# Kernel optimization log

Measured on AMD Instinct MI355X. Metric: run time of the kernel, lower is better.

The kernel has to match this reference:

```python
import jax, jax.numpy as jnp
import numpy as np

NUM_HEADS = 16
D_MODEL = 1024
NEG_INF = -1e30


def setup_inputs() -> dict:
    key = jax.random.key(0)
    ks = jax.random.split(key, 7)
    B, S, D = 2, 2048, D_MODEL
    scale = 1.0 / np.sqrt(D)
    return {
        "queries": jax.random.normal(ks[0], (B, S, D), dtype=jnp.float32),
        "keys": jax.random.normal(ks[1], (B, S, D), dtype=jnp.float32),
        "values": jax.random.normal(ks[2], (B, S, D), dtype=jnp.float32),
        "Wq": jax.random.normal(ks[3], (D, D), dtype=jnp.float32) * scale,
        "Wk": jax.random.normal(ks[4], (D, D), dtype=jnp.float32) * scale,
        "Wv": jax.random.normal(ks[5], (D, D), dtype=jnp.float32) * scale,
        "Wo": jax.random.normal(ks[6], (D, D), dtype=jnp.float32) * scale,
    }


def _split_heads(x, h):
    # [B, S, D] -> [B, h, S, D/h]
    B, S, D = x.shape
    return x.reshape(B, S, h, D // h).transpose(0, 2, 1, 3)


def reference(queries, keys, values, Wq, Wk, Wv, Wo):
    h = NUM_HEADS
    q = _split_heads(queries @ Wq, h)  # [B, h, S, dh]
    k = _split_heads(keys @ Wk, h)
    v = _split_heads(values @ Wv, h)
    dh = q.shape[-1]
    scores = jnp.einsum("bhqd,bhkd->bhqk", q, k) / jnp.sqrt(jnp.float32(dh))
    # original quirk: exactly-zero scores are masked to -1e30 before softmax
    scores = jnp.where(scores == 0, NEG_INF, scores)
    attn = jax.nn.softmax(scores, axis=-1)
    out = jnp.einsum("bhqk,bhkd->bhqd", attn, v)  # [B, h, S, dh]
    B, _, S, _ = out.shape
    out = out.transpose(0, 2, 1, 3).reshape(B, S, h * dh)
    return out @ Wo
```

## Files before the change

### kernel.cpp

```cpp
#include <hip/hip_runtime.h>
#include <math.h>

typedef unsigned short u16;
typedef short bf16x8 __attribute__((ext_vector_type(8)));
typedef float f32x4 __attribute__((ext_vector_type(4)));

namespace {

constexpr int kB = 2, kS = 2048, kD = 1024, kH = 16, kDh = 64;

__device__ inline u16 f32_bf16(float f) {
    unsigned u = __float_as_uint(f);
    u += 0x7FFFu + ((u >> 16) & 1u);
    return (u16)(u >> 16);
}

__device__ inline u16 f32_bf16_fast(float f) {
    return (u16)((__float_as_uint(f) + 0x8000u) >> 16);
}

__device__ inline void gl_lds16(const void* g, void* l) {
    __builtin_amdgcn_global_load_lds(
        (const __attribute__((address_space(1))) void*)g,
        (__attribute__((address_space(3))) void*)l, 16, 0, 0);
}

__global__ __launch_bounds__(256) void conv_bf16_3(
    const float* __restrict__ s0, const float* __restrict__ s1,
    const float* __restrict__ s2,
    u16* __restrict__ d0, u16* __restrict__ d1, u16* __restrict__ d2)
{
    const int z = blockIdx.y;
    const float* src = z == 0 ? s0 : (z == 1 ? s1 : s2);
    u16* dst = z == 0 ? d0 : (z == 1 ? d1 : d2);
    const int i = blockIdx.x * 256 + threadIdx.x;
    const float4* s4 = (const float4*)src;
    float4 a = s4[2 * i], b = s4[2 * i + 1];
    uint4 o;
    o.x = (unsigned)f32_bf16(a.x) | ((unsigned)f32_bf16(a.y) << 16);
    o.y = (unsigned)f32_bf16(a.z) | ((unsigned)f32_bf16(a.w) << 16);
    o.z = (unsigned)f32_bf16(b.x) | ((unsigned)f32_bf16(b.y) << 16);
    o.w = (unsigned)f32_bf16(b.z) | ((unsigned)f32_bf16(b.w) << 16);
    ((uint4*)dst)[i] = o;
}

__global__ __launch_bounds__(256) void wtrans4(
    const float* __restrict__ W0, const float* __restrict__ W1,
    const float* __restrict__ W2, const float* __restrict__ W3,
    u16* __restrict__ T0, u16* __restrict__ T1,
    u16* __restrict__ T2, u16* __restrict__ T3)
{
    const int z = blockIdx.z;
    const float* W = z == 0 ? W0 : (z == 1 ? W1 : (z == 2 ? W2 : W3));
    u16* Wt = z == 0 ? T0 : (z == 1 ? T1 : (z == 2 ? T2 : T3));

    __shared__ __attribute__((aligned(16))) u16 T[64][65];
    const int t = threadIdx.x;
    const int n0 = blockIdx.x * 64, k0 = blockIdx.y * 64;
    const int r = t >> 4, c4 = (t & 15) * 4;
#pragma unroll
    for (int it = 0; it < 4; ++it) {
        const int rr = r + 16 * it;
        float4 v = *(const float4*)(W + (size_t)(k0 + rr) * kD + n0 + c4);
        T[rr][c4 + 0] = f32_bf16(v.x);
        T[rr][c4 + 1] = f32_bf16(v.y);
        T[rr][c4 + 2] = f32_bf16(v.z);
        T[rr][c4 + 3] = f32_bf16(v.w);
    }
    __syncthreads();
#pragma unroll
    for (int it = 0; it < 4; ++it) {
        const int nn = r + 16 * it;
        uint2 pk;
        pk.x = (unsigned)T[c4 + 0][nn] | ((unsigned)T[c4 + 1][nn] << 16);
        pk.y = (unsigned)T[c4 + 2][nn] | ((unsigned)T[c4 + 3][nn] << 16);
        *(uint2*)(Wt + (size_t)(n0 + nn) * kD + k0 + c4) = pk;
    }
}

__global__ __launch_bounds__(256) void vtrans(
    const u16* __restrict__ V, u16* __restrict__ Vt)
{
    __shared__ __attribute__((aligned(16))) u16 T[64][65];
    const int t = threadIdx.x;
    const int s0 = blockIdx.x * 64;
    const int bh = blockIdx.y, b = bh >> 4, h = bh & 15;
    const int rr = t >> 3, c0 = (t & 7) * 8;
    union { u16 u[8]; uint4 v4; } buf;
#pragma unroll
    for (int p = 0; p < 2; ++p) {
        const int s = rr + 32 * p;
        buf.v4 = *(const uint4*)(V + (size_t)(b * kS + s0 + s) * kD + h * kDh + c0);
#pragma unroll
        for (int i = 0; i < 8; ++i) T[c0 + i][s] = buf.u[i];
    }
    __syncthreads();
#pragma unroll
    for (int p = 0; p < 2; ++p) {
        const int d = rr + 32 * p;
#pragma unroll
        for (int i = 0; i < 8; ++i) buf.u[i] = T[d][c0 + i];
        *(uint4*)(Vt + (size_t)(bh * kDh + d) * kS + s0 + c0) = buf.v4;
    }
}

template <bool F32OUT>
__device__ inline void gemm_body(
    const u16* __restrict__ A, const u16* __restrict__ Wt,
    void* __restrict__ Cout, int M, int N, int K, int bx, int by)
{
    __shared__ __attribute__((aligned(16))) u16 As[64 * 32];
    __shared__ __attribute__((aligned(16))) u16 Bs[128 * 32];
    const int t = threadIdx.x, w = t >> 6, l = t & 63;
    const int quad = l >> 4, c = l & 15;
    const int m0 = by * 64, n0 = bx * 128;
    const int lr = l >> 2, lc = (l & 3) * 8;

    const u16* ga  = A  + (size_t)(m0 + w * 16 + lr) * K + lc;
    const u16* gb0 = Wt + (size_t)(n0 + w * 16 + lr) * K + lc;
    const u16* gb1 = Wt + (size_t)(n0 + 64 + w * 16 + lr) * K + lc;
    u16* lda  = &As[w * 512];
    u16* ldb0 = &Bs[w * 512];
    u16* ldb1 = &Bs[2048 + w * 512];

    const int fa = c * 32 + quad * 8;
    const int fb = (w * 32 + c) * 32 + quad * 8;

    f32x4 acc[4][2];
#pragma unroll
    for (int mi = 0; mi < 4; ++mi)
#pragma unroll
        for (int nj = 0; nj < 2; ++nj) acc[mi][nj] = 0;

    for (int k0 = 0; k0 < K; k0 += 32) {
        gl_lds16(ga + k0, lda);
        gl_lds16(gb0 + k0, ldb0);
        gl_lds16(gb1 + k0, ldb1);
        __syncthreads();
        bf16x8 af[4], bf[2];
#pragma unroll
        for (int mi = 0; mi < 4; ++mi) af[mi] = *(const bf16x8*)&As[fa + mi * 512];
#pragma unroll
        for (int nj = 0; nj < 2; ++nj) bf[nj] = *(const bf16x8*)&Bs[fb + nj * 512];
#pragma unroll
        for (int mi = 0; mi < 4; ++mi)
#pragma unroll
            for (int nj = 0; nj < 2; ++nj)
                acc[mi][nj] = __builtin_amdgcn_mfma_f32_16x16x32_bf16(
                    af[mi], bf[nj], acc[mi][nj], 0, 0, 0);
        __syncthreads();
    }

#pragma unroll
    for (int mi = 0; mi < 4; ++mi)
#pragma unroll
        for (int nj = 0; nj < 2; ++nj)
#pragma unroll
            for (int r = 0; r < 4; ++r) {
                const size_t row = m0 + mi * 16 + quad * 4 + r;
                const size_t col = n0 + w * 32 + nj * 16 + c;
                if (F32OUT)
                    ((float*)Cout)[row * N + col] = acc[mi][nj][r];
                else
                    ((u16*)Cout)[row * N + col] = f32_bf16(acc[mi][nj][r]);
            }
}

__global__ __launch_bounds__(256) void gemm_qkv(
    const u16* __restrict__ A0, const u16* __restrict__ A1,
    const u16* __restrict__ A2,
    const u16* __restrict__ W0, const u16* __restrict__ W1,
    const u16* __restrict__ W2,
    u16* __restrict__ C0, u16* __restrict__ C1, u16* __restrict__ C2)
{
    const int z = blockIdx.z;
    const u16* A  = z == 0 ? A0 : (z == 1 ? A1 : A2);
    const u16* Wt = z == 0 ? W0 : (z == 1 ? W1 : W2);
    u16* C = z == 0 ? C0 : (z == 1 ? C1 : C2);
    gemm_body<false>(A, Wt, C, kB * kS, kD, kD, blockIdx.x, blockIdx.y);
}

__global__ __launch_bounds__(256) void gemm_out(
    const u16* __restrict__ A, const u16* __restrict__ Wt,
    float* __restrict__ C)
{
    gemm_body<true>(A, Wt, C, kB * kS, kD, kD, blockIdx.x, blockIdx.y);
}

__global__ __launch_bounds__(256) void attn(
    const u16* __restrict__ Q, const u16* __restrict__ K,
    const u16* __restrict__ Vt, u16* __restrict__ AO)
{
    __shared__ __attribute__((aligned(16))) u16 KsL[2 * 64 * 32];
    __shared__ __attribute__((aligned(16))) u16 VtL[2 * 64 * 32];
    __shared__ __attribute__((aligned(16))) u16 QPs[9216];

    const int t = threadIdx.x, w = t >> 6, l = t & 63;
    const int quad = l >> 4, c = l & 15;
    const int q0 = blockIdx.x * 128;
    const int bh = blockIdx.y, b = bh >> 4, h = bh & 15;
    const int lr = l >> 2, lc8 = (l & 3) * 8;

    const size_t qbase = (size_t)(b * kS + q0) * kD + h * kDh;
#pragma unroll
    for (int p = 0; p < 2; ++p)
#pragma unroll
        for (int hf = 0; hf < 2; ++hf) {
            const int r0 = w * 32 + hf * 16;
            gl_lds16(Q + qbase + (size_t)(r0 + lr) * kD + p * 32 + lc8,
                     &QPs[p * 4096 + r0 * 32]);
        }
    __syncthreads();

    bf16x8 qf[2][2];
#pragma unroll
    for (int mi = 0; mi < 2; ++mi)
#pragma unroll
        for (int p = 0; p < 2; ++p)
            qf[mi][p] = *(const bf16x8*)
                &QPs[p * 4096 + (w * 32 + mi * 16 + c) * 32 + quad * 8];

    f32x4 o[2][4];
    float l_run[2][4];
#pragma unroll
    for (int mi = 0; mi < 2; ++mi)
#pragma unroll
        for (int r = 0; r < 4; ++r) l_run[mi][r] = 0.0f;
#pragma unroll
    for (int mi = 0; mi < 2; ++mi)
#pragma unroll
        for (int nj = 0; nj < 4; ++nj) o[mi][nj] = 0;

    const size_t kbase = (size_t)(b * kS) * kD + h * kDh;
    const size_t vbase = (size_t)bh * kDh * kS;
    const int p_w = w >> 1, hf_w = w & 1;
    const float c2 = 0.125f * 1.44269504088896341f;

    for (int kt = 0; kt < kS / 64; ++kt) {
#pragma unroll
        for (int h2 = 0; h2 < 2; ++h2) {
            const int r0 = hf_w * 32 + h2 * 16;
            gl_lds16(K + kbase + (size_t)(kt * 64 + r0 + lr) * kD + p_w * 32 + lc8,
                     &KsL[p_w * 2048 + r0 * 32]);
            gl_lds16(Vt + vbase + (size_t)(r0 + lr) * kS + kt * 64 + p_w * 32 + lc8,
                     &VtL[p_w * 2048 + r0 * 32]);
        }
        __syncthreads();

        f32x4 s[2][4];
#pragma unroll
        for (int mi = 0; mi < 2; ++mi)
#pragma unroll
            for (int nj = 0; nj < 4; ++nj) s[mi][nj] = 0;
#pragma unroll
        for (int p = 0; p < 2; ++p) {
            bf16x8 bk[4];
#pragma unroll
            for (int nj = 0; nj < 4; ++nj)
                bk[nj] = *(const bf16x8*)&KsL[p * 2048 + (nj * 16 + c) * 32 + quad * 8];
#pragma unroll
            for (int mi = 0; mi < 2; ++mi)
#pragma unroll
                for (int nj = 0; nj < 4; ++nj)
                    s[mi][nj] = __builtin_amdgcn_mfma_f32_16x16x32_bf16(
                        qf[mi][p], bk[nj], s[mi][nj], 0, 0, 0);
        }

#pragma unroll
        for (int mi = 0; mi < 2; ++mi)
#pragma unroll
            for (int nj = 0; nj < 4; ++nj)
#pragma unroll
                for (int r = 0; r < 4; ++r) {
                    const float sv = s[mi][nj][r];
                    float p = exp2f(sv * c2);
                    p = (sv == 0.0f) ? 0.0f : p;
                    l_run[mi][r] += p;
                    QPs[w * 2304 + (mi * 16 + quad * 4 + r) * 72 + nj * 16 + c] =
                        f32_bf16_fast(p);
                }

#pragma unroll
        for (int kp = 0; kp < 2; ++kp) {
            bf16x8 pf[2], vf[4];
#pragma unroll
            for (int mi = 0; mi < 2; ++mi)
                pf[mi] = *(const bf16x8*)
                    &QPs[w * 2304 + (mi * 16 + c) * 72 + kp * 32 + quad * 8];
#pragma unroll
            for (int nj = 0; nj < 4; ++nj)
                vf[nj] = *(const bf16x8*)&VtL[kp * 2048 + (nj * 16 + c) * 32 + quad * 8];
#pragma unroll
            for (int mi = 0; mi < 2; ++mi)
#pragma unroll
                for (int nj = 0; nj < 4; ++nj)
                    o[mi][nj] = __builtin_amdgcn_mfma_f32_16x16x32_bf16(
                        pf[mi], vf[nj], o[mi][nj], 0, 0, 0);
        }
        __syncthreads();
    }

    const size_t obase = (size_t)(b * kS + q0 + w * 32) * kD + h * kDh;
#pragma unroll
    for (int mi = 0; mi < 2; ++mi)
#pragma unroll
        for (int r = 0; r < 4; ++r) {
            float lv = l_run[mi][r];
            lv += __shfl_xor(lv, 1);
            lv += __shfl_xor(lv, 2);
            lv += __shfl_xor(lv, 4);
            lv += __shfl_xor(lv, 8);
            const float inv = 1.0f / lv;
#pragma unroll
            for (int nj = 0; nj < 4; ++nj)
                AO[obase + (size_t)(mi * 16 + quad * 4 + r) * kD + nj * 16 + c] =
                    f32_bf16(o[mi][nj][r] * inv);
        }
}

}

extern "C" void kernel_launch(void* const* d_in, const int* in_sizes, int n_in,
                              void* d_out, int out_size, void* d_ws, size_t ws_size,
                              hipStream_t stream)
{
    const float* q_in = (const float*)d_in[0];
    const float* k_in = (const float*)d_in[1];
    const float* v_in = (const float*)d_in[2];
    const float* Wq   = (const float*)d_in[3];
    const float* Wk   = (const float*)d_in[4];
    const float* Wv   = (const float*)d_in[5];
    const float* Wo   = (const float*)d_in[6];

    u16* ws = (u16*)d_ws;
    const size_t M1 = 1u << 20;
    u16* xq  = ws;
    u16* xk  = ws + 4 * M1;
    u16* xv  = ws + 8 * M1;
    u16* Wtq = ws + 12 * M1;
    u16* Wtk = ws + 13 * M1;
    u16* Wtv = ws + 14 * M1;
    u16* Wto = ws + 15 * M1;
    u16* Qp  = ws + 16 * M1;
    u16* Kp  = ws + 20 * M1;
    u16* Vp  = ws + 24 * M1;
    u16* AO  = ws + 28 * M1;
    u16* Vtg = xq;

    hipLaunchKernelGGL(conv_bf16_3, dim3(2048, 3), dim3(256), 0, stream,
                       q_in, k_in, v_in, xq, xk, xv);

    hipLaunchKernelGGL(wtrans4, dim3(16, 16, 4), dim3(256), 0, stream,
                       Wq, Wk, Wv, Wo, Wtq, Wtk, Wtv, Wto);

    hipLaunchKernelGGL(gemm_qkv, dim3(8, 64, 3), dim3(256), 0, stream,
                       xq, xk, xv, Wtq, Wtk, Wtv, Qp, Kp, Vp);

    hipLaunchKernelGGL(vtrans, dim3(32, 32), dim3(256), 0, stream, Vp, Vtg);

    hipLaunchKernelGGL(attn, dim3(16, 32), dim3(256), 0, stream, Qp, Kp, Vtg, AO);

    hipLaunchKernelGGL(gemm_out, dim3(8, 64), dim3(256), 0, stream,
                       AO, Wto, (float*)d_out);
}
```

Before: 268.3 us.

## Enlarge GEMM tiles to 128x128, fold softmax scale into Wq, shrink attention tiles

The projection GEMMs move from 64x128 to 128x128 block tiles, with a 2x2 warp layout and 4x4 MFMA accumulators per warp, to raise data reuse per LDS load. The softmax scale and log2e factor are folded into Wq during weight conversion, which removes a multiply per score. The softmax row sum is now computed by an extra MFMA against a ones vector instead of scalar adds and shuffles. Attention blocks now cover 64 queries with 16 per warp, doubling the grid, which lowers per-block work and register use but loads K/V tiles twice as often. Folding the scale into bf16 Wq changes rounding and slightly changes which scores come out as exactly zero.

```diff
diff --git a/kernel.cpp b/kernel.cpp
--- a/kernel.cpp
+++ b/kernel.cpp
@@ -8,6 +8,7 @@
 namespace {
 
 constexpr int kB = 2, kS = 2048, kD = 1024, kH = 16, kDh = 64;
+constexpr float kC2 = 0.125f * 1.44269504088896341f;
 
 __device__ inline u16 f32_bf16(float f) {
     unsigned u = __float_as_uint(f);
@@ -53,6 +54,7 @@
     const int z = blockIdx.z;
     const float* W = z == 0 ? W0 : (z == 1 ? W1 : (z == 2 ? W2 : W3));
     u16* Wt = z == 0 ? T0 : (z == 1 ? T1 : (z == 2 ? T2 : T3));
+    const float sc = (z == 0) ? kC2 : 1.0f;
 
     __shared__ __attribute__((aligned(16))) u16 T[64][65];
     const int t = threadIdx.x;
@@ -62,10 +64,10 @@
     for (int it = 0; it < 4; ++it) {
         const int rr = r + 16 * it;
         float4 v = *(const float4*)(W + (size_t)(k0 + rr) * kD + n0 + c4);
-        T[rr][c4 + 0] = f32_bf16(v.x);
-        T[rr][c4 + 1] = f32_bf16(v.y);
-        T[rr][c4 + 2] = f32_bf16(v.z);
-        T[rr][c4 + 3] = f32_bf16(v.w);
+        T[rr][c4 + 0] = f32_bf16(v.x * sc);
+        T[rr][c4 + 1] = f32_bf16(v.y * sc);
+        T[rr][c4 + 2] = f32_bf16(v.z * sc);
+        T[rr][c4 + 3] = f32_bf16(v.w * sc);
     }
     __syncthreads();
 #pragma unroll
@@ -105,47 +107,50 @@
 }
 
 template <bool F32OUT>
-__device__ inline void gemm_body(
+__device__ inline void gemm128_body(
     const u16* __restrict__ A, const u16* __restrict__ Wt,
     void* __restrict__ Cout, int M, int N, int K, int bx, int by)
 {
-    __shared__ __attribute__((aligned(16))) u16 As[64 * 32];
+    __shared__ __attribute__((aligned(16))) u16 As[128 * 32];
     __shared__ __attribute__((aligned(16))) u16 Bs[128 * 32];
     const int t = threadIdx.x, w = t >> 6, l = t & 63;
     const int quad = l >> 4, c = l & 15;
-    const int m0 = by * 64, n0 = bx * 128;
+    const int wm = w >> 1, wn = w & 1;
+    const int m0 = by * 128, n0 = bx * 128;
     const int lr = l >> 2, lc = (l & 3) * 8;
 
-    const u16* ga  = A  + (size_t)(m0 + w * 16 + lr) * K + lc;
-    const u16* gb0 = Wt + (size_t)(n0 + w * 16 + lr) * K + lc;
-    const u16* gb1 = Wt + (size_t)(n0 + 64 + w * 16 + lr) * K + lc;
-    u16* lda  = &As[w * 512];
-    u16* ldb0 = &Bs[w * 512];
-    u16* ldb1 = &Bs[2048 + w * 512];
-
-    const int fa = c * 32 + quad * 8;
-    const int fb = (w * 32 + c) * 32 + quad * 8;
-
-    f32x4 acc[4][2];
+    const u16* ga0 = A  + (size_t)(m0 + w * 32 + lr) * K + lc;
+    const u16* ga1 = A  + (size_t)(m0 + w * 32 + 16 + lr) * K + lc;
+    const u16* gb0 = Wt + (size_t)(n0 + w * 32 + lr) * K + lc;
+    const u16* gb1 = Wt + (size_t)(n0 + w * 32 + 16 + lr) * K + lc;
+    u16* la0 = &As[(w * 32) * 32];
+    u16* la1 = &As[(w * 32 + 16) * 32];
+    u16* lb0 = &Bs[(w * 32) * 32];
+    u16* lb1 = &Bs[(w * 32 + 16) * 32];
+
+    f32x4 acc[4][4];
 #pragma unroll
     for (int mi = 0; mi < 4; ++mi)
 #pragma unroll
-        for (int nj = 0; nj < 2; ++nj) acc[mi][nj] = 0;
+        for (int nj = 0; nj < 4; ++nj) acc[mi][nj] = 0;
 
     for (int k0 = 0; k0 < K; k0 += 32) {
-        gl_lds16(ga + k0, lda);
-        gl_lds16(gb0 + k0, ldb0);
-        gl_lds16(gb1 + k0, ldb1);
+        gl_lds16(ga0 + k0, la0);
+        gl_lds16(ga1 + k0, la1);
+        gl_lds16(gb0 + k0, lb0);
+        gl_lds16(gb1 + k0, lb1);
         __syncthreads();
-        bf16x8 af[4], bf[2];
-#pragma unroll
-        for (int mi = 0; mi < 4; ++mi) af[mi] = *(const bf16x8*)&As[fa + mi * 512];
-#pragma unroll
-        for (int nj = 0; nj < 2; ++nj) bf[nj] = *(const bf16x8*)&Bs[fb + nj * 512];
+        bf16x8 af[4], bf[4];
 #pragma unroll
         for (int mi = 0; mi < 4; ++mi)
-#pragma unroll
-            for (int nj = 0; nj < 2; ++nj)
+            af[mi] = *(const bf16x8*)&As[(wm * 64 + mi * 16 + c) * 32 + quad * 8];
+#pragma unroll
+        for (int nj = 0; nj < 4; ++nj)
+            bf[nj] = *(const bf16x8*)&Bs[(wn * 64 + nj * 16 + c) * 32 + quad * 8];
+#pragma unroll
+        for (int mi = 0; mi < 4; ++mi)
+#pragma unroll
+            for (int nj = 0; nj < 4; ++nj)
                 acc[mi][nj] = __builtin_amdgcn_mfma_f32_16x16x32_bf16(
                     af[mi], bf[nj], acc[mi][nj], 0, 0, 0);
         __syncthreads();
@@ -154,11 +159,11 @@
 #pragma unroll
     for (int mi = 0; mi < 4; ++mi)
 #pragma unroll
-        for (int nj = 0; nj < 2; ++nj)
+        for (int nj = 0; nj < 4; ++nj)
 #pragma unroll
             for (int r = 0; r < 4; ++r) {
-                const size_t row = m0 + mi * 16 + quad * 4 + r;
-                const size_t col = n0 + w * 32 + nj * 16 + c;
+                const size_t row = m0 + wm * 64 + mi * 16 + quad * 4 + r;
+                const size_t col = n0 + wn * 64 + nj * 16 + c;
                 if (F32OUT)
                     ((float*)Cout)[row * N + col] = acc[mi][nj][r];
                 else
@@ -177,14 +182,14 @@
     const u16* A  = z == 0 ? A0 : (z == 1 ? A1 : A2);
     const u16* Wt = z == 0 ? W0 : (z == 1 ? W1 : W2);
     u16* C = z == 0 ? C0 : (z == 1 ? C1 : C2);
-    gemm_body<false>(A, Wt, C, kB * kS, kD, kD, blockIdx.x, blockIdx.y);
+    gemm128_body<false>(A, Wt, C, kB * kS, kD, kD, blockIdx.x, blockIdx.y);
 }
 
 __global__ __launch_bounds__(256) void gemm_out(
     const u16* __restrict__ A, const u16* __restrict__ Wt,
     float* __restrict__ C)
 {
-    gemm_body<true>(A, Wt, C, kB * kS, kD, kD, blockIdx.x, blockIdx.y);
+    gemm128_body<true>(A, Wt, C, kB * kS, kD, kD, blockIdx.x, blockIdx.y);
 }
 
 __global__ __launch_bounds__(256) void attn(
@@ -193,48 +198,39 @@
 {
     __shared__ __attribute__((aligned(16))) u16 KsL[2 * 64 * 32];
     __shared__ __attribute__((aligned(16))) u16 VtL[2 * 64 * 32];
-    __shared__ __attribute__((aligned(16))) u16 QPs[9216];
+    __shared__ __attribute__((aligned(16))) u16 Qs[2 * 64 * 32];
+    __shared__ __attribute__((aligned(16))) u16 Ps[4 * 16 * 72];
 
     const int t = threadIdx.x, w = t >> 6, l = t & 63;
     const int quad = l >> 4, c = l & 15;
-    const int q0 = blockIdx.x * 128;
+    const int q0 = blockIdx.x * 64;
     const int bh = blockIdx.y, b = bh >> 4, h = bh & 15;
     const int lr = l >> 2, lc8 = (l & 3) * 8;
 
     const size_t qbase = (size_t)(b * kS + q0) * kD + h * kDh;
 #pragma unroll
     for (int p = 0; p < 2; ++p)
-#pragma unroll
-        for (int hf = 0; hf < 2; ++hf) {
-            const int r0 = w * 32 + hf * 16;
-            gl_lds16(Q + qbase + (size_t)(r0 + lr) * kD + p * 32 + lc8,
-                     &QPs[p * 4096 + r0 * 32]);
-        }
+        gl_lds16(Q + qbase + (size_t)(w * 16 + lr) * kD + p * 32 + lc8,
+                 &Qs[p * 2048 + (w * 16) * 32]);
     __syncthreads();
 
-    bf16x8 qf[2][2];
-#pragma unroll
-    for (int mi = 0; mi < 2; ++mi)
-#pragma unroll
-        for (int p = 0; p < 2; ++p)
-            qf[mi][p] = *(const bf16x8*)
-                &QPs[p * 4096 + (w * 32 + mi * 16 + c) * 32 + quad * 8];
-
-    f32x4 o[2][4];
-    float l_run[2][4];
-#pragma unroll
-    for (int mi = 0; mi < 2; ++mi)
-#pragma unroll
-        for (int r = 0; r < 4; ++r) l_run[mi][r] = 0.0f;
-#pragma unroll
-    for (int mi = 0; mi < 2; ++mi)
-#pragma unroll
-        for (int nj = 0; nj < 4; ++nj) o[mi][nj] = 0;
+    bf16x8 qf[2];
+#pragma unroll
+    for (int p = 0; p < 2; ++p)
+        qf[p] = *(const bf16x8*)&Qs[p * 2048 + (w * 16 + c) * 32 + quad * 8];
+
+    bf16x8 ones;
+#pragma unroll
+    for (int i = 0; i < 8; ++i) ones[i] = (short)0x3F80;
+
+    f32x4 o[4], ol;
+#pragma unroll
+    for (int nj = 0; nj < 4; ++nj) o[nj] = 0;
+    ol = 0;
 
     const size_t kbase = (size_t)(b * kS) * kD + h * kDh;
     const size_t vbase = (size_t)bh * kDh * kS;
     const int p_w = w >> 1, hf_w = w & 1;
-    const float c2 = 0.125f * 1.44269504088896341f;
 
     for (int kt = 0; kt < kS / 64; ++kt) {
 #pragma unroll
@@ -247,75 +243,55 @@
         }
         __syncthreads();
 
-        f32x4 s[2][4];
-#pragma unroll
-        for (int mi = 0; mi < 2; ++mi)
-#pragma unroll
-            for (int nj = 0; nj < 4; ++nj) s[mi][nj] = 0;
+        f32x4 s[4];
+#pragma unroll
+        for (int nj = 0; nj < 4; ++nj) s[nj] = 0;
 #pragma unroll
         for (int p = 0; p < 2; ++p) {
-            bf16x8 bk[4];
-#pragma unroll
-            for (int nj = 0; nj < 4; ++nj)
-                bk[nj] = *(const bf16x8*)&KsL[p * 2048 + (nj * 16 + c) * 32 + quad * 8];
-#pragma unroll
-            for (int mi = 0; mi < 2; ++mi)
-#pragma unroll
-                for (int nj = 0; nj < 4; ++nj)
-                    s[mi][nj] = __builtin_amdgcn_mfma_f32_16x16x32_bf16(
-                        qf[mi][p], bk[nj], s[mi][nj], 0, 0, 0);
+#pragma unroll
+            for (int nj = 0; nj < 4; ++nj) {
+                const bf16x8 bk =
+                    *(const bf16x8*)&KsL[p * 2048 + (nj * 16 + c) * 32 + quad * 8];
+                s[nj] = __builtin_amdgcn_mfma_f32_16x16x32_bf16(
+                    qf[p], bk, s[nj], 0, 0, 0);
+            }
         }
 
 #pragma unroll
-        for (int mi = 0; mi < 2; ++mi)
-#pragma unroll
-            for (int nj = 0; nj < 4; ++nj)
-#pragma unroll
-                for (int r = 0; r < 4; ++r) {
-                    const float sv = s[mi][nj][r];
-                    float p = exp2f(sv * c2);
-                    p = (sv == 0.0f) ? 0.0f : p;
-                    l_run[mi][r] += p;
-                    QPs[w * 2304 + (mi * 16 + quad * 4 + r) * 72 + nj * 16 + c] =
-                        f32_bf16_fast(p);
-                }
+        for (int nj = 0; nj < 4; ++nj)
+#pragma unroll
+            for (int r = 0; r < 4; ++r) {
+                const float sv = s[nj][r];
+                float p = exp2f(sv);
+                p = (sv == 0.0f) ? 0.0f : p;
+                Ps[w * 1152 + (quad * 4 + r) * 72 + nj * 16 + c] = f32_bf16_fast(p);
+            }
 
 #pragma unroll
         for (int kp = 0; kp < 2; ++kp) {
-            bf16x8 pf[2], vf[4];
-#pragma unroll
-            for (int mi = 0; mi < 2; ++mi)
-                pf[mi] = *(const bf16x8*)
-                    &QPs[w * 2304 + (mi * 16 + c) * 72 + kp * 32 + quad * 8];
-#pragma unroll
-            for (int nj = 0; nj < 4; ++nj)
-                vf[nj] = *(const bf16x8*)&VtL[kp * 2048 + (nj * 16 + c) * 32 + quad * 8];
-#pragma unroll
-            for (int mi = 0; mi < 2; ++mi)
-#pragma unroll
-                for (int nj = 0; nj < 4; ++nj)
-                    o[mi][nj] = __builtin_amdgcn_mfma_f32_16x16x32_bf16(
-                        pf[mi], vf[nj], o[mi][nj], 0, 0, 0);
+            const bf16x8 pf =
+                *(const bf16x8*)&Ps[w * 1152 + c * 72 + kp * 32 + quad * 8];
+#pragma unroll
+            for (int nj = 0; nj < 4; ++nj) {
+                const bf16x8 vf =
+                    *(const bf16x8*)&VtL[kp * 2048 + (nj * 16 + c) * 32 + quad * 8];
+                o[nj] = __builtin_amdgcn_mfma_f32_16x16x32_bf16(
+                    pf, vf, o[nj], 0, 0, 0);
+            }
+            ol = __builtin_amdgcn_mfma_f32_16x16x32_bf16(pf, ones, ol, 0, 0, 0);
         }
         __syncthreads();
     }
 
-    const size_t obase = (size_t)(b * kS + q0 + w * 32) * kD + h * kDh;
-#pragma unroll
-    for (int mi = 0; mi < 2; ++mi)
-#pragma unroll
-        for (int r = 0; r < 4; ++r) {
-            float lv = l_run[mi][r];
-            lv += __shfl_xor(lv, 1);
-            lv += __shfl_xor(lv, 2);
-            lv += __shfl_xor(lv, 4);
-            lv += __shfl_xor(lv, 8);
-            const float inv = 1.0f / lv;
-#pragma unroll
-            for (int nj = 0; nj < 4; ++nj)
-                AO[obase + (size_t)(mi * 16 + quad * 4 + r) * kD + nj * 16 + c] =
-                    f32_bf16(o[mi][nj][r] * inv);
-        }
+    const size_t obase = (size_t)(b * kS + q0 + w * 16) * kD + h * kDh;
+#pragma unroll
+    for (int r = 0; r < 4; ++r) {
+        const float inv = 1.0f / ol[r];
+#pragma unroll
+        for (int nj = 0; nj < 4; ++nj)
+            AO[obase + (size_t)(quad * 4 + r) * kD + nj * 16 + c] =
+                f32_bf16(o[nj][r] * inv);
+    }
 }
 
 }
@@ -353,13 +329,13 @@
     hipLaunchKernelGGL(wtrans4, dim3(16, 16, 4), dim3(256), 0, stream,
                        Wq, Wk, Wv, Wo, Wtq, Wtk, Wtv, Wto);
 
-    hipLaunchKernelGGL(gemm_qkv, dim3(8, 64, 3), dim3(256), 0, stream,
+    hipLaunchKernelGGL(gemm_qkv, dim3(8, 32, 3), dim3(256), 0, stream,
                        xq, xk, xv, Wtq, Wtk, Wtv, Qp, Kp, Vp);
 
     hipLaunchKernelGGL(vtrans, dim3(32, 32), dim3(256), 0, stream, Vp, Vtg);
 
-    hipLaunchKernelGGL(attn, dim3(16, 32), dim3(256), 0, stream, Qp, Kp, Vtg, AO);
-
-    hipLaunchKernelGGL(gemm_out, dim3(8, 64), dim3(256), 0, stream,
+    hipLaunchKernelGGL(attn, dim3(32, 32), dim3(256), 0, stream, Qp, Kp, Vtg, AO);
+
+    hipLaunchKernelGGL(gemm_out, dim3(8, 32), dim3(256), 0, stream,
                        AO, Wto, (float*)d_out);
 }
```

After: 259.3 us. 1.03x faster.
